# Performance work log

Hardware: AMD Instinct MI355X
Metric: run time of the kernel (lower is better)

## Reference

```python
import jax, jax.numpy as jnp
import numpy as np

T, H, F, E, K = 2048, 1024, 1024, 8, 2  # tokens, hidden, ffn, experts, top_k


def setup_inputs() -> dict:
    key = jax.random.key(0)
    k1, k2, k3, k4, k5 = jax.random.split(key, 5)
    hidden_states = jax.random.normal(k1, (T, H), dtype=jnp.float32)
    # router outputs: positive weights (renormalize=False in module, used as-is)
    topk_weights = jax.random.uniform(k2, (T, K), dtype=jnp.float32)
    topk_ids = jax.random.randint(k3, (T, K), 0, E, dtype=jnp.int32)
    # gate_up: (E, 2F, H) with first F rows = gate, last F rows = up
    gate_up_weight = jax.random.normal(k4, (E, 2 * F, H), dtype=jnp.float32) * 0.02
    # down: (E, H, F)
    down_weight = jax.random.normal(k5, (E, H, F), dtype=jnp.float32) * 0.02
    return {
        'hidden_states': hidden_states,
        'topk_weights': topk_weights,
        'topk_ids': topk_ids,
        'gate_up_weight': gate_up_weight,
        'down_weight': down_weight,
    }


def reference(hidden_states, topk_weights, topk_ids, gate_up_weight, down_weight):
    # Fused MoE: per selected expert, y = (silu(x@Wg^T) * (x@Wu^T)) @ Wd^T,
    # combined with router weights (renormalize=False).
    f = down_weight.shape[-1]
    # [T, E, 2F]: gate_up projection for every expert (dense ref for grouped GEMM)
    gu = jnp.einsum('th,eoh->teo', hidden_states, gate_up_weight)
    gate, up = gu[..., :f], gu[..., f:]
    act = jax.nn.silu(gate) * up                     # [T, E, F]
    y = jnp.einsum('tef,ehf->teh', act, down_weight)  # [T, E, H]
    # gather the top-k experts per token and combine
    y_sel = jnp.take_along_axis(y, topk_ids[:, :, None], axis=1)  # [T, K, H]
    out = jnp.sum(y_sel * topk_weights[:, :, None], axis=1)       # [T, H]
    return out.astype(hidden_states.dtype)
```

## Files before the change

kernel.cpp:

```cpp
#include <hip/hip_runtime.h>
#include <hip/hip_bf16.h>

#define T_TOK 2048
#define HID   1024
#define FF    1024
#define NEXP  8
#define NPAIR 4096

#define BM 128
#define BK 32
#define MAX_MT 40
#define MAXROWS (MAX_MT*BM)
#define PPT (NPAIR/256)

using bf16x8 = __attribute__((ext_vector_type(8))) __bf16;
using f32x4  = __attribute__((ext_vector_type(4))) float;

__device__ __forceinline__ unsigned short f2bf(float f) {
    unsigned int u = __float_as_uint(f);
    return (unsigned short)((u + 0x7FFF + ((u >> 16) & 1)) >> 16);
}
__device__ __forceinline__ float bf2f(unsigned short s) {
    return __uint_as_float(((unsigned int)s) << 16);
}
__device__ __forceinline__ void gll16(const unsigned short* g, unsigned short* l) {
    __builtin_amdgcn_global_load_lds(
        (const __attribute__((address_space(1))) void*)(const void*)g,
        (__attribute__((address_space(3))) void*)(void*)l, 16, 0, 0);
}

__global__ void prep_kernel(const float* __restrict__ wgu,
                            const float* __restrict__ wdn,
                            const float* __restrict__ hs,
                            const int* __restrict__ ids,
                            int* __restrict__ pair_pos,
                            int* __restrict__ row_tok,
                            int* __restrict__ meta,
                            unsigned short* __restrict__ wgu_b,
                            unsigned short* __restrict__ wdn_b,
                            unsigned short* __restrict__ hs_b) {
    int tid = threadIdx.x;
    if (blockIdx.x == 2048) {
        __shared__ int S[2][256][NEXP];
        __shared__ int base[NEXP];
        int myc[NEXP];
        int eloc[PPT];
#pragma unroll
        for (int e = 0; e < NEXP; e++) myc[e] = 0;
#pragma unroll
        for (int i = 0; i < PPT; i++) {
            int e = ids[tid * PPT + i];
            eloc[i] = e;
#pragma unroll
            for (int ee = 0; ee < NEXP; ee++) myc[ee] += (e == ee);
        }
#pragma unroll
        for (int e = 0; e < NEXP; e++) S[0][tid][e] = myc[e];
        __syncthreads();
        int src = 0;
        for (int d = 1; d < 256; d <<= 1) {
#pragma unroll
            for (int e = 0; e < NEXP; e++) {
                int v = S[src][tid][e];
                if (tid >= d) v += S[src][tid - d][e];
                S[src ^ 1][tid][e] = v;
            }
            __syncthreads();
            src ^= 1;
        }
        if (tid == 0) {
            int mt = 0;
            for (int e = 0; e < NEXP; e++) {
                meta[e] = mt;
                base[e] = mt * BM;
                mt += (S[src][255][e] + BM - 1) / BM;
            }
            meta[NEXP] = mt;
        }
        for (int i = tid; i < MAXROWS; i += 256) row_tok[i] = -1;
        __syncthreads();
        int off[NEXP];
#pragma unroll
        for (int e = 0; e < NEXP; e++) off[e] = base[e] + S[src][tid][e] - myc[e];
#pragma unroll
        for (int i = 0; i < PPT; i++) {
            int p = tid * PPT + i;
            int e = eloc[i];
            int pos = 0;
#pragma unroll
            for (int ee = 0; ee < NEXP; ee++) if (e == ee) pos = off[ee]++;
            pair_pos[p] = pos;
            row_tok[pos] = p >> 1;
        }
        return;
    }
    long stride = 2048L * 256;
    long t0 = (long)blockIdx.x * 256 + tid;
    const long NW1 = (long)NEXP * 2 * FF * HID / 4;
    for (long i = t0; i < NW1; i += stride) {
        float4 v = ((const float4*)wgu)[i];
        ushort4 o; o.x = f2bf(v.x); o.y = f2bf(v.y); o.z = f2bf(v.z); o.w = f2bf(v.w);
        ((ushort4*)wgu_b)[i] = o;
    }
    const long NW2 = (long)NEXP * HID * FF / 4;
    for (long i = t0; i < NW2; i += stride) {
        float4 v = ((const float4*)wdn)[i];
        ushort4 o; o.x = f2bf(v.x); o.y = f2bf(v.y); o.z = f2bf(v.z); o.w = f2bf(v.w);
        ((ushort4*)wdn_b)[i] = o;
    }
    const long NH = (long)T_TOK * HID / 4;
    for (long i = t0; i < NH; i += stride) {
        float4 v = ((const float4*)hs)[i];
        ushort4 o; o.x = f2bf(v.x); o.y = f2bf(v.y); o.z = f2bf(v.z); o.w = f2bf(v.w);
        ((ushort4*)hs_b)[i] = o;
    }
}

template<int EPI, int NBY, int BN>
__global__ __launch_bounds__(256)
void gemm_moe(const unsigned short* __restrict__ A,
              const unsigned short* __restrict__ B,
              unsigned short* __restrict__ Cbf,
              const int* __restrict__ meta,
              const int* __restrict__ row_tok,
              int K, long Bexp) {
    constexpr int NJ = BN / 32;
    constexpr int NBCH = (BN * BK) / (8 * 256);
    __shared__ unsigned short As[2][BM * BK];
    __shared__ unsigned short Bs[2][BN * BK];

    int L = blockIdx.x;
    int xcd = L & 7;
    int slot = L >> 3;
    constexpr int PER = NBY / 8;
    int by = xcd * PER + (slot % PER);
    int bx = slot / PER;
    if (bx >= meta[NEXP]) return;
    int e = 0;
#pragma unroll
    for (int i = 1; i < NEXP; i++) if (bx >= meta[i]) e = i;

    long m0 = (long)bx * BM;
    int n0 = by * BN;
    const unsigned short* Bb = B + (long)e * Bexp;

    int tid = threadIdx.x, lane = tid & 63, wv = tid >> 6;
    const int r = lane & 15;
    const int q = lane >> 4;
    const int mw = (wv >> 1) * 64, nw = (wv & 1) * (BN / 2);
    const int sw = (q ^ ((r >> 1) & 3)) * 8;

    const unsigned short* ap[2];
#pragma unroll
    for (int h = 0; h < 2; h++) {
        int c = h * 256 + tid;
        int row = c >> 2, cp = c & 3;
        int cc = cp ^ ((row >> 1) & 3);
        long grow;
        if (EPI == 1) {
            int tk = row_tok[m0 + row];
            if (tk < 0) tk = 0;
            grow = tk;
        } else {
            grow = m0 + row;
        }
        ap[h] = A + grow * (long)K + cc * 8;
    }
    const unsigned short* bp[NBCH];
#pragma unroll
    for (int h = 0; h < NBCH; h++) {
        int c = h * 256 + tid;
        int row = c >> 2, cp = c & 3;
        int cc = cp ^ ((row >> 1) & 3);
        long grow;
        if (EPI == 1) grow = ((row & 1) ? FF : 0) + ((n0 + row) >> 1);
        else          grow = n0 + row;
        bp[h] = Bb + grow * (long)K + cc * 8;
    }

    auto stage = [&](int s, int k0) {
#pragma unroll
        for (int h = 0; h < 2; h++)
            gll16(ap[h] + k0, &As[s][(h * 256 + tid) * 8]);
#pragma unroll
        for (int h = 0; h < NBCH; h++)
            gll16(bp[h] + k0, &Bs[s][(h * 256 + tid) * 8]);
    };

    f32x4 acc[4][NJ] = {};
    const int NKI = K / BK;
    stage(0, 0);
    for (int ki = 0; ki < NKI; ki++) {
        __syncthreads();
        if (ki + 1 < NKI) stage((ki + 1) & 1, (ki + 1) * BK);
        int s = ki & 1;
        bf16x8 a[4], b[NJ];
#pragma unroll
        for (int i = 0; i < 4; i++)
            a[i] = *(const bf16x8*)&As[s][(mw + i * 16 + r) * BK + sw];
#pragma unroll
        for (int j = 0; j < NJ; j++)
            b[j] = *(const bf16x8*)&Bs[s][(nw + j * 16 + r) * BK + sw];
#pragma unroll
        for (int i = 0; i < 4; i++)
#pragma unroll
            for (int j = 0; j < NJ; j++)
                acc[i][j] = __builtin_amdgcn_mfma_f32_16x16x32_bf16(a[i], b[j], acc[i][j], 0, 0, 0);
        __syncthreads();
    }

    if (EPI == 1) {
#pragma unroll
        for (int i = 0; i < 4; i++) {
            long rowb = m0 + mw + i * 16 + q * 4;
#pragma unroll
            for (int j = 0; j < NJ; j++) {
                int n = n0 + nw + j * 16 + r;
#pragma unroll
                for (int reg = 0; reg < 4; reg++) {
                    float v = acc[i][j][reg];
                    float o = __shfl_xor(v, 1);
                    if (!(r & 1)) {
                        float g = v, u = o;
                        float s2 = g / (1.f + __expf(-g)) * u;
                        Cbf[(rowb + reg) * (long)FF + (n >> 1)] = f2bf(s2);
                    }
                }
            }
        }
    } else {
#pragma unroll
        for (int i = 0; i < 4; i++) {
            long rowb = m0 + mw + i * 16 + q * 4;
#pragma unroll
            for (int j = 0; j < NJ; j++) {
                int n = n0 + nw + j * 16 + r;
#pragma unroll
                for (int reg = 0; reg < 4; reg++)
                    Cbf[(rowb + reg) * (long)HID + n] = f2bf(acc[i][j][reg]);
            }
        }
    }
}

__global__ void combine_kernel(const unsigned short* __restrict__ y,
                               const float* __restrict__ tw,
                               const int* __restrict__ pair_pos,
                               float* __restrict__ out) {
    int t = blockIdx.x;
    int c = threadIdx.x * 4;
    int p0 = pair_pos[t * 2], p1 = pair_pos[t * 2 + 1];
    float w0 = tw[t * 2], w1 = tw[t * 2 + 1];
    ushort4 a = *(const ushort4*)(y + (long)p0 * HID + c);
    ushort4 b = *(const ushort4*)(y + (long)p1 * HID + c);
    float4 o;
    o.x = w0 * bf2f(a.x) + w1 * bf2f(b.x);
    o.y = w0 * bf2f(a.y) + w1 * bf2f(b.y);
    o.z = w0 * bf2f(a.z) + w1 * bf2f(b.z);
    o.w = w0 * bf2f(a.w) + w1 * bf2f(b.w);
    *(float4*)(out + (long)t * HID + c) = o;
}

extern "C" void kernel_launch(void* const* d_in, const int* in_sizes, int n_in,
                              void* d_out, int out_size, void* d_ws, size_t ws_size,
                              hipStream_t stream) {
    const float* hs  = (const float*)d_in[0];
    const float* tw  = (const float*)d_in[1];
    const int*   ids = (const int*)d_in[2];
    const float* wgu = (const float*)d_in[3];
    const float* wdn = (const float*)d_in[4];
    float* out = (float*)d_out;

    char* ws = (char*)d_ws;
    size_t off = 0;
    auto alloc = [&](size_t bytes) -> void* {
        void* p = ws + off;
        off += (bytes + 255) & ~(size_t)255;
        return p;
    };
    unsigned short* wgu_b = (unsigned short*)alloc((size_t)NEXP * 2 * FF * HID * 2);
    unsigned short* wdn_b = (unsigned short*)alloc((size_t)NEXP * HID * FF * 2);
    unsigned short* hs_b  = (unsigned short*)alloc((size_t)T_TOK * HID * 2);
    unsigned short* act   = (unsigned short*)alloc((size_t)MAXROWS * FF * 2);
    unsigned short* ybuf  = (unsigned short*)alloc((size_t)MAXROWS * HID * 2);
    int* pair_pos = (int*)alloc(NPAIR * 4);
    int* row_tok  = (int*)alloc(MAXROWS * 4);
    int* meta     = (int*)alloc(64);

    prep_kernel<<<2049, 256, 0, stream>>>(wgu, wdn, hs, ids,
                                          pair_pos, row_tok, meta,
                                          wgu_b, wdn_b, hs_b);

    gemm_moe<1, 16, 128><<<16 * MAX_MT, 256, 0, stream>>>(
        hs_b, wgu_b, act, meta, row_tok, HID, (long)(2 * FF) * HID);

    gemm_moe<2, 8, 128><<<8 * MAX_MT, 256, 0, stream>>>(
        act, wdn_b, ybuf, meta, row_tok, FF, (long)HID * FF);

    combine_kernel<<<T_TOK, 256, 0, stream>>>(ybuf, tw, pair_pos, out);
}
```

Before: 203.5 us.

## Fuse fp32-to-bf16 weight conversion into GEMM B-tile loads

Result: slower. 220.9 us (+8.5%).

```diff
diff --git a/kernel.cpp b/kernel.cpp
--- a/kernel.cpp
+++ b/kernel.cpp
@@ -15,6 +15,7 @@
 
 using bf16x8 = __attribute__((ext_vector_type(8))) __bf16;
 using f32x4  = __attribute__((ext_vector_type(4))) float;
+using us8    = __attribute__((ext_vector_type(8))) unsigned short;
 
 __device__ __forceinline__ unsigned short f2bf(float f) {
     unsigned int u = __float_as_uint(f);
@@ -29,18 +30,14 @@
         (__attribute__((address_space(3))) void*)(void*)l, 16, 0, 0);
 }
 
-__global__ void prep_kernel(const float* __restrict__ wgu,
-                            const float* __restrict__ wdn,
-                            const float* __restrict__ hs,
+__global__ void prep_kernel(const float* __restrict__ hs,
                             const int* __restrict__ ids,
                             int* __restrict__ pair_pos,
                             int* __restrict__ row_tok,
                             int* __restrict__ meta,
-                            unsigned short* __restrict__ wgu_b,
-                            unsigned short* __restrict__ wdn_b,
                             unsigned short* __restrict__ hs_b) {
     int tid = threadIdx.x;
-    if (blockIdx.x == 2048) {
+    if (blockIdx.x == 1024) {
         __shared__ int S[2][256][NEXP];
         __shared__ int base[NEXP];
         int myc[NEXP];
@@ -94,20 +91,8 @@
         }
         return;
     }
-    long stride = 2048L * 256;
+    long stride = 1024L * 256;
     long t0 = (long)blockIdx.x * 256 + tid;
-    const long NW1 = (long)NEXP * 2 * FF * HID / 4;
-    for (long i = t0; i < NW1; i += stride) {
-        float4 v = ((const float4*)wgu)[i];
-        ushort4 o; o.x = f2bf(v.x); o.y = f2bf(v.y); o.z = f2bf(v.z); o.w = f2bf(v.w);
-        ((ushort4*)wgu_b)[i] = o;
-    }
-    const long NW2 = (long)NEXP * HID * FF / 4;
-    for (long i = t0; i < NW2; i += stride) {
-        float4 v = ((const float4*)wdn)[i];
-        ushort4 o; o.x = f2bf(v.x); o.y = f2bf(v.y); o.z = f2bf(v.z); o.w = f2bf(v.w);
-        ((ushort4*)wdn_b)[i] = o;
-    }
     const long NH = (long)T_TOK * HID / 4;
     for (long i = t0; i < NH; i += stride) {
         float4 v = ((const float4*)hs)[i];
@@ -119,7 +104,7 @@
 template<int EPI, int NBY, int BN>
 __global__ __launch_bounds__(256)
 void gemm_moe(const unsigned short* __restrict__ A,
-              const unsigned short* __restrict__ B,
+              const float* __restrict__ B,
               unsigned short* __restrict__ Cbf,
               const int* __restrict__ meta,
               const int* __restrict__ row_tok,
@@ -142,7 +127,7 @@
 
     long m0 = (long)bx * BM;
     int n0 = by * BN;
-    const unsigned short* Bb = B + (long)e * Bexp;
+    const float* Bb = B + (long)e * Bexp;
 
     int tid = threadIdx.x, lane = tid & 63, wv = tid >> 6;
     const int r = lane & 15;
@@ -166,7 +151,7 @@
         }
         ap[h] = A + grow * (long)K + cc * 8;
     }
-    const unsigned short* bp[NBCH];
+    const float* bp[NBCH];
 #pragma unroll
     for (int h = 0; h < NBCH; h++) {
         int c = h * 256 + tid;
@@ -178,22 +163,43 @@
         bp[h] = Bb + grow * (long)K + cc * 8;
     }
 
-    auto stage = [&](int s, int k0) {
+    float4 br[NBCH][2];
+    auto bload = [&](int k0) {
+#pragma unroll
+        for (int h = 0; h < NBCH; h++) {
+            br[h][0] = *(const float4*)(bp[h] + k0);
+            br[h][1] = *(const float4*)(bp[h] + k0 + 4);
+        }
+    };
+    auto bwrite = [&](int s) {
+#pragma unroll
+        for (int h = 0; h < NBCH; h++) {
+            us8 o;
+            o[0] = f2bf(br[h][0].x); o[1] = f2bf(br[h][0].y);
+            o[2] = f2bf(br[h][0].z); o[3] = f2bf(br[h][0].w);
+            o[4] = f2bf(br[h][1].x); o[5] = f2bf(br[h][1].y);
+            o[6] = f2bf(br[h][1].z); o[7] = f2bf(br[h][1].w);
+            *(us8*)&Bs[s][(h * 256 + tid) * 8] = o;
+        }
+    };
+    auto stageA = [&](int s, int k0) {
 #pragma unroll
         for (int h = 0; h < 2; h++)
             gll16(ap[h] + k0, &As[s][(h * 256 + tid) * 8]);
-#pragma unroll
-        for (int h = 0; h < NBCH; h++)
-            gll16(bp[h] + k0, &Bs[s][(h * 256 + tid) * 8]);
     };
 
     f32x4 acc[4][NJ] = {};
     const int NKI = K / BK;
-    stage(0, 0);
+    bload(0);
+    stageA(0, 0);
+    bwrite(0);
     for (int ki = 0; ki < NKI; ki++) {
         __syncthreads();
-        if (ki + 1 < NKI) stage((ki + 1) & 1, (ki + 1) * BK);
         int s = ki & 1;
+        if (ki + 1 < NKI) {
+            bload((ki + 1) * BK);
+            stageA(s ^ 1, (ki + 1) * BK);
+        }
         bf16x8 a[4], b[NJ];
 #pragma unroll
         for (int i = 0; i < 4; i++)
@@ -206,6 +212,7 @@
 #pragma unroll
             for (int j = 0; j < NJ; j++)
                 acc[i][j] = __builtin_amdgcn_mfma_f32_16x16x32_bf16(a[i], b[j], acc[i][j], 0, 0, 0);
+        if (ki + 1 < NKI) bwrite(s ^ 1);
         __syncthreads();
     }
 
@@ -278,8 +285,6 @@
         off += (bytes + 255) & ~(size_t)255;
         return p;
     };
-    unsigned short* wgu_b = (unsigned short*)alloc((size_t)NEXP * 2 * FF * HID * 2);
-    unsigned short* wdn_b = (unsigned short*)alloc((size_t)NEXP * HID * FF * 2);
     unsigned short* hs_b  = (unsigned short*)alloc((size_t)T_TOK * HID * 2);
     unsigned short* act   = (unsigned short*)alloc((size_t)MAXROWS * FF * 2);
     unsigned short* ybuf  = (unsigned short*)alloc((size_t)MAXROWS * HID * 2);
@@ -287,15 +292,13 @@
     int* row_tok  = (int*)alloc(MAXROWS * 4);
     int* meta     = (int*)alloc(64);
 
-    prep_kernel<<<2049, 256, 0, stream>>>(wgu, wdn, hs, ids,
-                                          pair_pos, row_tok, meta,
-                                          wgu_b, wdn_b, hs_b);
+    prep_kernel<<<1025, 256, 0, stream>>>(hs, ids, pair_pos, row_tok, meta, hs_b);
 
     gemm_moe<1, 16, 128><<<16 * MAX_MT, 256, 0, stream>>>(
-        hs_b, wgu_b, act, meta, row_tok, HID, (long)(2 * FF) * HID);
+        hs_b, wgu, act, meta, row_tok, HID, (long)(2 * FF) * HID);
 
     gemm_moe<2, 8, 128><<<8 * MAX_MT, 256, 0, stream>>>(
-        act, wdn_b, ybuf, meta, row_tok, FF, (long)HID * FF);
+        act, wdn, ybuf, meta, row_tok, FF, (long)HID * FF);
 
     combine_kernel<<<T_TOK, 256, 0, stream>>>(ybuf, tw, pair_pos, out);
 }
```

## Overlap down-weight bf16 conversion with first grouped GEMM via extra blocks

Applied to the files above, without the earlier changes.

Result: slower. 207.8 us (+2.1%).

```diff
diff --git a/kernel.cpp b/kernel.cpp
--- a/kernel.cpp
+++ b/kernel.cpp
@@ -28,16 +28,18 @@
         (const __attribute__((address_space(1))) void*)(const void*)g,
         (__attribute__((address_space(3))) void*)(void*)l, 16, 0, 0);
 }
+__device__ __forceinline__ ushort4 cvt4(float4 v) {
+    ushort4 o; o.x = f2bf(v.x); o.y = f2bf(v.y); o.z = f2bf(v.z); o.w = f2bf(v.w);
+    return o;
+}
 
 __global__ void prep_kernel(const float* __restrict__ wgu,
-                            const float* __restrict__ wdn,
                             const float* __restrict__ hs,
                             const int* __restrict__ ids,
                             int* __restrict__ pair_pos,
                             int* __restrict__ row_tok,
                             int* __restrict__ meta,
                             unsigned short* __restrict__ wgu_b,
-                            unsigned short* __restrict__ wdn_b,
                             unsigned short* __restrict__ hs_b) {
     int tid = threadIdx.x;
     if (blockIdx.x == 2048) {
@@ -97,39 +99,47 @@
     long stride = 2048L * 256;
     long t0 = (long)blockIdx.x * 256 + tid;
     const long NW1 = (long)NEXP * 2 * FF * HID / 4;
-    for (long i = t0; i < NW1; i += stride) {
-        float4 v = ((const float4*)wgu)[i];
-        ushort4 o; o.x = f2bf(v.x); o.y = f2bf(v.y); o.z = f2bf(v.z); o.w = f2bf(v.w);
-        ((ushort4*)wgu_b)[i] = o;
-    }
-    const long NW2 = (long)NEXP * HID * FF / 4;
-    for (long i = t0; i < NW2; i += stride) {
-        float4 v = ((const float4*)wdn)[i];
-        ushort4 o; o.x = f2bf(v.x); o.y = f2bf(v.y); o.z = f2bf(v.z); o.w = f2bf(v.w);
-        ((ushort4*)wdn_b)[i] = o;
+    const long H1 = NW1 / 2;
+    for (long i = t0; i < H1; i += stride) {
+        float4 v0 = ((const float4*)wgu)[i];
+        float4 v1 = ((const float4*)wgu)[i + H1];
+        ((ushort4*)wgu_b)[i]      = cvt4(v0);
+        ((ushort4*)wgu_b)[i + H1] = cvt4(v1);
     }
     const long NH = (long)T_TOK * HID / 4;
     for (long i = t0; i < NH; i += stride) {
         float4 v = ((const float4*)hs)[i];
-        ushort4 o; o.x = f2bf(v.x); o.y = f2bf(v.y); o.z = f2bf(v.z); o.w = f2bf(v.w);
-        ((ushort4*)hs_b)[i] = o;
-    }
-}
-
-template<int EPI, int NBY, int BN>
+        ((ushort4*)hs_b)[i] = cvt4(v);
+    }
+}
+
+template<int EPI, int NBY, int BN, int CONV>
 __global__ __launch_bounds__(256)
 void gemm_moe(const unsigned short* __restrict__ A,
               const unsigned short* __restrict__ B,
               unsigned short* __restrict__ Cbf,
               const int* __restrict__ meta,
               const int* __restrict__ row_tok,
-              int K, long Bexp) {
+              int K, long Bexp,
+              const float* __restrict__ Wsrc,
+              unsigned short* __restrict__ Wdst, long Wn4) {
     constexpr int NJ = BN / 32;
     constexpr int NBCH = (BN * BK) / (8 * 256);
     __shared__ unsigned short As[2][BM * BK];
     __shared__ unsigned short Bs[2][BN * BK];
 
+    int tid = threadIdx.x;
     int L = blockIdx.x;
+    if (CONV > 0 && L >= NBY * MAX_MT) {
+        long t0 = (long)(L - NBY * MAX_MT) * 256 + tid;
+        long stride = (long)CONV * 256;
+        for (long i = t0; i < Wn4; i += stride) {
+            float4 v = ((const float4*)Wsrc)[i];
+            ((ushort4*)Wdst)[i] = cvt4(v);
+        }
+        return;
+    }
+
     int xcd = L & 7;
     int slot = L >> 3;
     constexpr int PER = NBY / 8;
@@ -144,7 +154,7 @@
     int n0 = by * BN;
     const unsigned short* Bb = B + (long)e * Bexp;
 
-    int tid = threadIdx.x, lane = tid & 63, wv = tid >> 6;
+    int lane = tid & 63, wv = tid >> 6;
     const int r = lane & 15;
     const int q = lane >> 4;
     const int mw = (wv >> 1) * 64, nw = (wv & 1) * (BN / 2);
@@ -287,15 +297,17 @@
     int* row_tok  = (int*)alloc(MAXROWS * 4);
     int* meta     = (int*)alloc(64);
 
-    prep_kernel<<<2049, 256, 0, stream>>>(wgu, wdn, hs, ids,
-                                          pair_pos, row_tok, meta,
-                                          wgu_b, wdn_b, hs_b);
-
-    gemm_moe<1, 16, 128><<<16 * MAX_MT, 256, 0, stream>>>(
-        hs_b, wgu_b, act, meta, row_tok, HID, (long)(2 * FF) * HID);
-
-    gemm_moe<2, 8, 128><<<8 * MAX_MT, 256, 0, stream>>>(
-        act, wdn_b, ybuf, meta, row_tok, FF, (long)HID * FF);
+    prep_kernel<<<2049, 256, 0, stream>>>(wgu, hs, ids, pair_pos, row_tok, meta,
+                                          wgu_b, hs_b);
+
+    const long Wn4 = (long)NEXP * HID * FF / 4;
+    gemm_moe<1, 16, 128, 256><<<16 * MAX_MT + 256, 256, 0, stream>>>(
+        hs_b, wgu_b, act, meta, row_tok, HID, (long)(2 * FF) * HID,
+        wdn, wdn_b, Wn4);
+
+    gemm_moe<2, 8, 128, 0><<<8 * MAX_MT, 256, 0, stream>>>(
+        act, wdn_b, ybuf, meta, row_tok, FF, (long)HID * FF,
+        nullptr, nullptr, 0);
 
     combine_kernel<<<T_TOK, 256, 0, stream>>>(ybuf, tw, pair_pos, out);
 }
```

## Flatten fp32-to-bf16 conversion grid and halve M tile for down GEMM

Applied to the files above, without the earlier changes.

New measurement: 204.9 us. No clear change (+0.7%).

```diff
diff --git a/kernel.cpp b/kernel.cpp
--- a/kernel.cpp
+++ b/kernel.cpp
@@ -7,10 +7,9 @@
 #define NEXP  8
 #define NPAIR 4096
 
-#define BM 128
 #define BK 32
 #define MAX_MT 40
-#define MAXROWS (MAX_MT*BM)
+#define MAXROWS (MAX_MT*128)
 #define PPT (NPAIR/256)
 
 using bf16x8 = __attribute__((ext_vector_type(8))) __bf16;
@@ -28,6 +27,15 @@
         (const __attribute__((address_space(1))) void*)(const void*)g,
         (__attribute__((address_space(3))) void*)(void*)l, 16, 0, 0);
 }
+__device__ __forceinline__ ushort4 cvt4(float4 v) {
+    ushort4 o; o.x = f2bf(v.x); o.y = f2bf(v.y); o.z = f2bf(v.z); o.w = f2bf(v.w);
+    return o;
+}
+
+#define B_WGU 4096
+#define B_WDN 2048
+#define B_HS  512
+#define B_TOT (B_WGU + B_WDN + B_HS)
 
 __global__ void prep_kernel(const float* __restrict__ wgu,
                             const float* __restrict__ wdn,
@@ -40,83 +48,82 @@
                             unsigned short* __restrict__ wdn_b,
                             unsigned short* __restrict__ hs_b) {
     int tid = threadIdx.x;
-    if (blockIdx.x == 2048) {
-        __shared__ int S[2][256][NEXP];
-        __shared__ int base[NEXP];
-        int myc[NEXP];
-        int eloc[PPT];
-#pragma unroll
-        for (int e = 0; e < NEXP; e++) myc[e] = 0;
-#pragma unroll
-        for (int i = 0; i < PPT; i++) {
-            int e = ids[tid * PPT + i];
-            eloc[i] = e;
-#pragma unroll
-            for (int ee = 0; ee < NEXP; ee++) myc[ee] += (e == ee);
-        }
-#pragma unroll
-        for (int e = 0; e < NEXP; e++) S[0][tid][e] = myc[e];
+    int bid = blockIdx.x;
+    if (bid < B_TOT) {
+        const float4* src;
+        ushort4* dst;
+        long base;
+        if (bid < B_WGU) {
+            src = (const float4*)wgu; dst = (ushort4*)wgu_b;
+            base = (long)bid * 1024 + tid;
+        } else if (bid < B_WGU + B_WDN) {
+            src = (const float4*)wdn; dst = (ushort4*)wdn_b;
+            base = (long)(bid - B_WGU) * 1024 + tid;
+        } else {
+            src = (const float4*)hs; dst = (ushort4*)hs_b;
+            base = (long)(bid - B_WGU - B_WDN) * 1024 + tid;
+        }
+        float4 v[4];
+#pragma unroll
+        for (int k = 0; k < 4; k++) v[k] = src[base + k * 256];
+#pragma unroll
+        for (int k = 0; k < 4; k++) dst[base + k * 256] = cvt4(v[k]);
+        return;
+    }
+    __shared__ int S[2][256][NEXP];
+    __shared__ int base[NEXP];
+    int myc[NEXP];
+    int eloc[PPT];
+#pragma unroll
+    for (int e = 0; e < NEXP; e++) myc[e] = 0;
+#pragma unroll
+    for (int i = 0; i < PPT; i++) {
+        int e = ids[tid * PPT + i];
+        eloc[i] = e;
+#pragma unroll
+        for (int ee = 0; ee < NEXP; ee++) myc[ee] += (e == ee);
+    }
+#pragma unroll
+    for (int e = 0; e < NEXP; e++) S[0][tid][e] = myc[e];
+    __syncthreads();
+    int src = 0;
+    for (int d = 1; d < 256; d <<= 1) {
+#pragma unroll
+        for (int e = 0; e < NEXP; e++) {
+            int v = S[src][tid][e];
+            if (tid >= d) v += S[src][tid - d][e];
+            S[src ^ 1][tid][e] = v;
+        }
         __syncthreads();
-        int src = 0;
-        for (int d = 1; d < 256; d <<= 1) {
-#pragma unroll
-            for (int e = 0; e < NEXP; e++) {
-                int v = S[src][tid][e];
-                if (tid >= d) v += S[src][tid - d][e];
-                S[src ^ 1][tid][e] = v;
-            }
-            __syncthreads();
-            src ^= 1;
-        }
-        if (tid == 0) {
-            int mt = 0;
-            for (int e = 0; e < NEXP; e++) {
-                meta[e] = mt;
-                base[e] = mt * BM;
-                mt += (S[src][255][e] + BM - 1) / BM;
-            }
-            meta[NEXP] = mt;
-        }
-        for (int i = tid; i < MAXROWS; i += 256) row_tok[i] = -1;
-        __syncthreads();
-        int off[NEXP];
-#pragma unroll
-        for (int e = 0; e < NEXP; e++) off[e] = base[e] + S[src][tid][e] - myc[e];
-#pragma unroll
-        for (int i = 0; i < PPT; i++) {
-            int p = tid * PPT + i;
-            int e = eloc[i];
-            int pos = 0;
-#pragma unroll
-            for (int ee = 0; ee < NEXP; ee++) if (e == ee) pos = off[ee]++;
-            pair_pos[p] = pos;
-            row_tok[pos] = p >> 1;
-        }
-        return;
-    }
-    long stride = 2048L * 256;
-    long t0 = (long)blockIdx.x * 256 + tid;
-    const long NW1 = (long)NEXP * 2 * FF * HID / 4;
-    for (long i = t0; i < NW1; i += stride) {
-        float4 v = ((const float4*)wgu)[i];
-        ushort4 o; o.x = f2bf(v.x); o.y = f2bf(v.y); o.z = f2bf(v.z); o.w = f2bf(v.w);
-        ((ushort4*)wgu_b)[i] = o;
-    }
-    const long NW2 = (long)NEXP * HID * FF / 4;
-    for (long i = t0; i < NW2; i += stride) {
-        float4 v = ((const float4*)wdn)[i];
-        ushort4 o; o.x = f2bf(v.x); o.y = f2bf(v.y); o.z = f2bf(v.z); o.w = f2bf(v.w);
-        ((ushort4*)wdn_b)[i] = o;
-    }
-    const long NH = (long)T_TOK * HID / 4;
-    for (long i = t0; i < NH; i += stride) {
-        float4 v = ((const float4*)hs)[i];
-        ushort4 o; o.x = f2bf(v.x); o.y = f2bf(v.y); o.z = f2bf(v.z); o.w = f2bf(v.w);
-        ((ushort4*)hs_b)[i] = o;
-    }
-}
-
-template<int EPI, int NBY, int BN>
+        src ^= 1;
+    }
+    if (tid == 0) {
+        int mt = 0;
+        for (int e = 0; e < NEXP; e++) {
+            meta[e] = mt;
+            base[e] = mt * 128;
+            mt += (S[src][255][e] + 127) / 128;
+        }
+        meta[NEXP] = mt;
+    }
+    for (int i = tid; i < MAXROWS; i += 256) row_tok[i] = -1;
+    __syncthreads();
+    int off[NEXP];
+#pragma unroll
+    for (int e = 0; e < NEXP; e++) off[e] = base[e] + S[src][tid][e] - myc[e];
+#pragma unroll
+    for (int i = 0; i < PPT; i++) {
+        int p = tid * PPT + i;
+        int e = eloc[i];
+        int pos = 0;
+#pragma unroll
+        for (int ee = 0; ee < NEXP; ee++) if (e == ee) pos = off[ee]++;
+        pair_pos[p] = pos;
+        row_tok[pos] = p >> 1;
+    }
+}
+
+template<int EPI, int NBY, int BMt, int BN>
 __global__ __launch_bounds__(256)
 void gemm_moe(const unsigned short* __restrict__ A,
               const unsigned short* __restrict__ B,
@@ -124,35 +131,40 @@
               const int* __restrict__ meta,
               const int* __restrict__ row_tok,
               int K, long Bexp) {
+    constexpr int NI = BMt / 32;
     constexpr int NJ = BN / 32;
+    constexpr int ACH = (BMt * BK) / (8 * 256);
     constexpr int NBCH = (BN * BK) / (8 * 256);
-    __shared__ unsigned short As[2][BM * BK];
+    __shared__ unsigned short As[2][BMt * BK];
     __shared__ unsigned short Bs[2][BN * BK];
 
+    int tid = threadIdx.x;
     int L = blockIdx.x;
     int xcd = L & 7;
     int slot = L >> 3;
     constexpr int PER = NBY / 8;
     int by = xcd * PER + (slot % PER);
     int bx = slot / PER;
-    if (bx >= meta[NEXP]) return;
+    constexpr int SUB = 128 / BMt;
+    if (bx >= meta[NEXP] * SUB) return;
+    int bx128 = bx / SUB;
     int e = 0;
 #pragma unroll
-    for (int i = 1; i < NEXP; i++) if (bx >= meta[i]) e = i;
-
-    long m0 = (long)bx * BM;
+    for (int i = 1; i < NEXP; i++) if (bx128 >= meta[i]) e = i;
+
+    long m0 = (long)bx * BMt;
     int n0 = by * BN;
     const unsigned short* Bb = B + (long)e * Bexp;
 
-    int tid = threadIdx.x, lane = tid & 63, wv = tid >> 6;
+    int lane = tid & 63, wv = tid >> 6;
     const int r = lane & 15;
     const int q = lane >> 4;
-    const int mw = (wv >> 1) * 64, nw = (wv & 1) * (BN / 2);
+    const int mw = (wv >> 1) * (BMt / 2), nw = (wv & 1) * (BN / 2);
     const int sw = (q ^ ((r >> 1) & 3)) * 8;
 
-    const unsigned short* ap[2];
-#pragma unroll
-    for (int h = 0; h < 2; h++) {
+    const unsigned short* ap[ACH];
+#pragma unroll
+    for (int h = 0; h < ACH; h++) {
         int c = h * 256 + tid;
         int row = c >> 2, cp = c & 3;
         int cc = cp ^ ((row >> 1) & 3);
@@ -180,29 +192,29 @@
 
     auto stage = [&](int s, int k0) {
 #pragma unroll
-        for (int h = 0; h < 2; h++)
+        for (int h = 0; h < ACH; h++)
             gll16(ap[h] + k0, &As[s][(h * 256 + tid) * 8]);
 #pragma unroll
         for (int h = 0; h < NBCH; h++)
             gll16(bp[h] + k0, &Bs[s][(h * 256 + tid) * 8]);
     };
 
-    f32x4 acc[4][NJ] = {};
+    f32x4 acc[NI][NJ] = {};
     const int NKI = K / BK;
     stage(0, 0);
     for (int ki = 0; ki < NKI; ki++) {
         __syncthreads();
         if (ki + 1 < NKI) stage((ki + 1) & 1, (ki + 1) * BK);
         int s = ki & 1;
-        bf16x8 a[4], b[NJ];
-#pragma unroll
-        for (int i = 0; i < 4; i++)
+        bf16x8 a[NI], b[NJ];
+#pragma unroll
+        for (int i = 0; i < NI; i++)
             a[i] = *(const bf16x8*)&As[s][(mw + i * 16 + r) * BK + sw];
 #pragma unroll
         for (int j = 0; j < NJ; j++)
             b[j] = *(const bf16x8*)&Bs[s][(nw + j * 16 + r) * BK + sw];
 #pragma unroll
-        for (int i = 0; i < 4; i++)
+        for (int i = 0; i < NI; i++)
 #pragma unroll
             for (int j = 0; j < NJ; j++)
                 acc[i][j] = __builtin_amdgcn_mfma_f32_16x16x32_bf16(a[i], b[j], acc[i][j], 0, 0, 0);
@@ -211,7 +223,7 @@
 
     if (EPI == 1) {
 #pragma unroll
-        for (int i = 0; i < 4; i++) {
+        for (int i = 0; i < NI; i++) {
             long rowb = m0 + mw + i * 16 + q * 4;
 #pragma unroll
             for (int j = 0; j < NJ; j++) {
@@ -230,7 +242,7 @@
         }
     } else {
 #pragma unroll
-        for (int i = 0; i < 4; i++) {
+        for (int i = 0; i < NI; i++) {
             long rowb = m0 + mw + i * 16 + q * 4;
 #pragma unroll
             for (int j = 0; j < NJ; j++) {
@@ -287,14 +299,14 @@
     int* row_tok  = (int*)alloc(MAXROWS * 4);
     int* meta     = (int*)alloc(64);
 
-    prep_kernel<<<2049, 256, 0, stream>>>(wgu, wdn, hs, ids,
-                                          pair_pos, row_tok, meta,
-                                          wgu_b, wdn_b, hs_b);
-
-    gemm_moe<1, 16, 128><<<16 * MAX_MT, 256, 0, stream>>>(
+    prep_kernel<<<B_TOT + 1, 256, 0, stream>>>(wgu, wdn, hs, ids,
+                                               pair_pos, row_tok, meta,
+                                               wgu_b, wdn_b, hs_b);
+
+    gemm_moe<1, 16, 128, 128><<<16 * MAX_MT, 256, 0, stream>>>(
         hs_b, wgu_b, act, meta, row_tok, HID, (long)(2 * FF) * HID);
 
-    gemm_moe<2, 8, 128><<<8 * MAX_MT, 256, 0, stream>>>(
+    gemm_moe<2, 8, 64, 128><<<8 * (2 * MAX_MT), 256, 0, stream>>>(
         act, wdn_b, ybuf, meta, row_tok, FF, (long)HID * FF);
 
     combine_kernel<<<T_TOK, 256, 0, stream>>>(ybuf, tw, pair_pos, out);
```
